# Optimization experiments

Measured on AMD Instinct MI355X. Metric: run time of the kernel, lower is better.

The kernel has to match this reference:

```python
import jax, jax.numpy as jnp
import numpy as np

B, SEQ, C, H, L = 2, 512, 768, 12, 6
OBS = ACT = GOAL = 64
MAXEP = 1000
D = C // H
T3 = 3 * SEQ  # stacked (z, state, action) tokens per timestep


def _ln(x, g, b):
    m = jnp.mean(x, -1, keepdims=True)
    v = jnp.mean((x - m) ** 2, -1, keepdims=True)
    return (x - m) * jax.lax.rsqrt(v + 1e-5) * g + b


def setup_inputs() -> dict:
    key = jax.random.key(0)
    it = iter(jax.random.split(key, 64))
    nrm = lambda shape, s=0.02: jax.random.normal(next(it), shape, jnp.float32) * s
    z = lambda *s: jnp.zeros(s, jnp.float32)
    o = lambda *s: jnp.ones(s, jnp.float32)
    return dict(
        states=jax.random.normal(next(it), (B, SEQ, OBS), jnp.float32),
        actions=jax.random.normal(next(it), (B, SEQ, ACT), jnp.float32),
        goals=jax.random.normal(next(it), (B, 1, GOAL), jnp.float32),
        traj_mask=jnp.ones((B, SEQ), bool),
        timesteps=jax.random.randint(next(it), (B, SEQ), 0, MAXEP),
        W_s=nrm((OBS, C)), b_s=z(C),
        W_a=nrm((ACT, C)), b_a=z(C),
        W_g=nrm((GOAL, C)), b_g=z(C),
        E_t=nrm((MAXEP, C)),
        ln0_g=o(C), ln0_b=z(C),
        Wq=nrm((L, C, C)), bq=z(L, C),
        Wk=nrm((L, C, C)), bk=z(L, C),
        Wv=nrm((L, C, C)), bv=z(L, C),
        Wp=nrm((L, C, C)), bp=z(L, C),
        ln1_g=o(L, C), ln1_b=z(L, C),
        W1=nrm((L, C, 4 * C)), b1=z(L, 4 * C),
        W2=nrm((L, 4 * C, C)), b2=z(L, C),
        ln2_g=o(L, C), ln2_b=z(L, C),
        W_ps=nrm((C, OBS)), b_ps=z(OBS),
        W_pa=nrm((C, ACT)), b_pa=z(ACT),
    )


def _forward(states, actions, goals, timesteps,
             W_s, b_s, W_a, b_a, W_g, b_g, E_t, ln0_g, ln0_b,
             Wq, bq, Wk, bk, Wv, bv, Wp, bp, ln1_g, ln1_b,
             W1, b1, W2, b2, ln2_g, ln2_b, W_ps, b_ps, W_pa, b_pa):
    te = E_t[timesteps]  # [B,SEQ,C] time embeddings (use_pe_as_timestep path)
    s_emb = states @ W_s + b_s + te
    a_emb = actions @ W_a + b_a + te
    g = jnp.broadcast_to(goals, (goals.shape[0], SEQ, goals.shape[2]))
    z_emb = g @ W_g + b_g + te  # GOAL_CONDITION path
    # interleave (z, s, a) per timestep -> [B, 3*SEQ, C]
    x = jnp.stack((z_emb, s_emb, a_emb), axis=2).reshape(states.shape[0], T3, C)
    x = _ln(x, ln0_g, ln0_b)
    mask = jnp.tril(jnp.ones((T3, T3), bool))
    scale = 1.0 / np.sqrt(D)
    for l in range(L):
        q = (x @ Wq[l] + bq[l]).reshape(-1, T3, H, D)
        k = (x @ Wk[l] + bk[l]).reshape(-1, T3, H, D)
        v = (x @ Wv[l] + bv[l]).reshape(-1, T3, H, D)
        sc = jnp.einsum('bqhd,bkhd->bhqk', q, k) * scale
        sc = jnp.where(mask, sc, -jnp.inf)
        w = jax.nn.softmax(sc, axis=-1)
        att = jnp.einsum('bhqk,bkhd->bqhd', w, v).reshape(-1, T3, C)
        x = x + att @ Wp[l] + bp[l]
        x = _ln(x, ln1_g[l], ln1_b[l])
        h = jax.nn.gelu(x @ W1[l] + b1[l], approximate=False)
        x = x + h @ W2[l] + b2[l]
        x = _ln(x, ln2_g[l], ln2_b[l])
    x = x.reshape(-1, SEQ, 3, C)
    state_preds = x[:, :, 2] @ W_ps + b_ps     # read off action-token positions
    action_preds = jnp.tanh(x[:, :, 1] @ W_pa + b_pa)  # state-token positions
    return jnp.stack((state_preds, action_preds))  # [2,B,SEQ,64]


def reference(states, actions, goals, traj_mask, timesteps,
              W_s, b_s, W_a, b_a, W_g, b_g, E_t, ln0_g, ln0_b,
              Wq, bq, Wk, bk, Wv, bv, Wp, bp, ln1_g, ln1_b,
              W1, b1, W2, b2, ln2_g, ln2_b, W_ps, b_ps, W_pa, b_pa):
    del traj_mask  # unused on the GOAL_CONDITION path
    return _forward(states, actions, goals, timesteps,
                    W_s, b_s, W_a, b_a, W_g, b_g, E_t, ln0_g, ln0_b,
                    Wq, bq, Wk, bk, Wv, bv, Wp, bp, ln1_g, ln1_b,
                    W1, b1, W2, b2, ln2_g, ln2_b, W_ps, b_ps, W_pa, b_pa)
```

## Files before the change

### kernel.cpp

```cpp
#include <hip/hip_runtime.h>

#define SEQ 512
#define T3 1536
#define CDIM 768
#define NH 12
#define HD 64
#define NL 6

typedef __attribute__((ext_vector_type(8))) short bh8;
typedef __attribute__((ext_vector_type(4))) short s4;
typedef __attribute__((ext_vector_type(4))) float f4;

__device__ inline short f2bf(float f) {
    union { float f; unsigned u; } x; x.f = f;
    unsigned r = x.u + 0x7FFFu + ((x.u >> 16) & 1u);
    return (short)(r >> 16);
}

__device__ inline float bf2f(short s) {
    union { unsigned u; float f; } x;
    x.u = ((unsigned)(unsigned short)s) << 16;
    return x.f;
}

__device__ inline void gload16(const short* g, const short* l) {
    __builtin_amdgcn_global_load_lds(
        (const __attribute__((address_space(1))) unsigned int*)g,
        (__attribute__((address_space(3))) unsigned int*)l, 16, 0, 0);
}

__device__ inline float block_sum(float v, volatile float* red, int tid) {
    #pragma unroll
    for (int off = 32; off > 0; off >>= 1) v += __shfl_down(v, off, 64);
    __syncthreads();
    if ((tid & 63) == 0) red[tid >> 6] = v;
    __syncthreads();
    return red[0] + red[1] + red[2] + red[3];
}

__global__ __launch_bounds__(256) void conv64_k(
        const float* __restrict__ Wq, const float* __restrict__ Wk,
        const float* __restrict__ Wv, const float* __restrict__ Wp,
        const float* __restrict__ W1, const float* __restrict__ W2,
        short* __restrict__ dst, int l0) {
    int flat = blockIdx.x;
    int lrel = flat / 1728, r = flat - lrel * 1728;
    int l = l0 + lrel;
    short* dstL = dst + (size_t)lrel * 7077888;
    const float* src; short* d; int K, N, tk, tn;
    if (r < 576) {
        int mat = r / 144, t = r - mat * 144;
        tk = t / 12; tn = t % 12; K = 768; N = 768;
        const float* srcs[4] = {Wq, Wk, Wv, Wp};
        src = srcs[mat] + (size_t)l * 589824;
        d = dstL + mat * 589824;
    } else if (r < 1152) {
        int t = r - 576; tk = t / 48; tn = t % 48; K = 768; N = 3072;
        src = W1 + (size_t)l * 2359296; d = dstL + 2359296;
    } else {
        int t = r - 1152; tk = t / 12; tn = t % 12; K = 3072; N = 768;
        src = W2 + (size_t)l * 2359296; d = dstL + 4718592;
    }
    int k0 = tk * 64, n0 = tn * 64;
    __shared__ float t2[64][65];
    int tid = threadIdx.x;
    int rk = tid >> 4, cn4 = (tid & 15) * 4;
    #pragma unroll
    for (int p = 0; p < 4; ++p) {
        f4 v = *(const f4*)(src + (size_t)(k0 + p * 16 + rk) * N + n0 + cn4);
        #pragma unroll
        for (int j = 0; j < 4; ++j) t2[cn4 + j][p * 16 + rk] = v[j];
    }
    __syncthreads();
    int n = tid >> 2, kb = (tid & 3) * 16;
    bh8 o0, o1;
    #pragma unroll
    for (int j = 0; j < 8; ++j) o0[j] = f2bf(t2[n][kb + j]);
    #pragma unroll
    for (int j = 0; j < 8; ++j) o1[j] = f2bf(t2[n][kb + 8 + j]);
    short* wp = d + (size_t)(n0 + n) * K + k0 + kb;
    *(bh8*)wp = o0;
    *(bh8*)(wp + 8) = o1;
}

__global__ __launch_bounds__(256) void embed_ln0_k(
        const float* __restrict__ states, const float* __restrict__ actions,
        const float* __restrict__ goals, const int* __restrict__ timesteps,
        const float* __restrict__ W_s, const float* __restrict__ b_s,
        const float* __restrict__ W_a, const float* __restrict__ b_a,
        const float* __restrict__ W_g, const float* __restrict__ b_g,
        const float* __restrict__ E_t, const float* __restrict__ g0,
        const float* __restrict__ bb0, float* __restrict__ x, short* __restrict__ xb) {
    int row = blockIdx.x;
    int b = row / T3, t3 = row - b * T3;
    int t = t3 / 3, kind = t3 - t * 3;
    __shared__ float inv[64];
    __shared__ float xr[CDIM];
    __shared__ float red[4];
    int tid = threadIdx.x;
    const float* src; const float* W; const float* bias;
    if (kind == 0)      { src = goals + b * 64;                       W = W_g; bias = b_g; }
    else if (kind == 1) { src = states + ((size_t)b * SEQ + t) * 64;  W = W_s; bias = b_s; }
    else                { src = actions + ((size_t)b * SEQ + t) * 64; W = W_a; bias = b_a; }
    if (tid < 64) inv[tid] = src[tid];
    __syncthreads();
    int ts = timesteps[b * SEQ + t];
    for (int c = tid; c < CDIM; c += 256) {
        float acc = bias[c] + E_t[(size_t)ts * CDIM + c];
        #pragma unroll 8
        for (int kk = 0; kk < 64; ++kk) acc += inv[kk] * W[kk * CDIM + c];
        xr[c] = acc;
    }
    __syncthreads();
    float v0 = xr[tid], v1 = xr[tid + 256], v2 = xr[tid + 512];
    float mean = block_sum(v0 + v1 + v2, red, tid) * (1.f / CDIM);
    float d0 = v0 - mean, d1 = v1 - mean, d2 = v2 - mean;
    float var = block_sum(d0 * d0 + d1 * d1 + d2 * d2, red, tid) * (1.f / CDIM);
    float rs = rsqrtf(var + 1e-5f);
    float* w = x + (size_t)row * CDIM;
    short* wb = xb + (size_t)row * CDIM;
    float o0 = d0 * rs * g0[tid]       + bb0[tid];
    float o1 = d1 * rs * g0[tid + 256] + bb0[tid + 256];
    float o2 = d2 * rs * g0[tid + 512] + bb0[tid + 512];
    w[tid] = o0; w[tid + 256] = o1; w[tid + 512] = o2;
    wb[tid] = f2bf(o0); wb[tid + 256] = f2bf(o1); wb[tid + 512] = f2bf(o2);
}

__global__ __launch_bounds__(256) void ln_k(float* __restrict__ x, short* __restrict__ outb,
                                            const float* __restrict__ g, const float* __restrict__ bb) {
    int row = blockIdx.x, tid = threadIdx.x;
    __shared__ float red[4];
    float* r = x + (size_t)row * CDIM;
    float v0 = r[tid], v1 = r[tid + 256], v2 = r[tid + 512];
    float mean = block_sum(v0 + v1 + v2, red, tid) * (1.f / CDIM);
    float d0 = v0 - mean, d1 = v1 - mean, d2 = v2 - mean;
    float var = block_sum(d0 * d0 + d1 * d1 + d2 * d2, red, tid) * (1.f / CDIM);
    float rs = rsqrtf(var + 1e-5f);
    short* wb = outb + (size_t)row * CDIM;
    float o0 = d0 * rs * g[tid]       + bb[tid];
    float o1 = d1 * rs * g[tid + 256] + bb[tid + 256];
    float o2 = d2 * rs * g[tid + 512] + bb[tid + 512];
    r[tid] = o0; r[tid + 256] = o1; r[tid + 512] = o2;
    wb[tid] = f2bf(o0); wb[tid + 256] = f2bf(o1); wb[tid + 512] = f2bf(o2);
}

template<int BM, int EPI>
__global__ __launch_bounds__(256) void gemm4_k(
        const short* __restrict__ A, const short* __restrict__ B0,
        const short* __restrict__ B1, const short* __restrict__ B2,
        const float* __restrict__ bias0, const float* __restrict__ bias1,
        const float* __restrict__ bias2,
        float* __restrict__ outF, short* __restrict__ outQ,
        short* __restrict__ outK, short* __restrict__ outV,
        int N, int K) {
    const short* Bw = B0; const float* bias = bias0; short* outB = outQ;
    int zid = 0;
    if (EPI == 0) {
        zid = blockIdx.z;
        if (zid == 1) { Bw = B1; bias = bias1; outB = outK; }
        else if (zid == 2) { Bw = B2; bias = bias2; outB = outV; }
    }
    __shared__ short As[2][BM * 64];
    __shared__ short Bs[2][128 * 64];
    int tid = threadIdx.x, lane = tid & 63, wave = tid >> 6;
    int wm = wave >> 1, wn = wave & 1, lr = lane & 15, lg = lane >> 4;
    int bm = blockIdx.y * BM, bn = blockIdx.x * 128;
    int rl = lane >> 3, ch = (lane & 7) ^ rl;
    constexpr int MI = BM / 32;

    auto STAGE = [&](int k0, int buf) {
        #pragma unroll
        for (int j = 0; j < BM / 32; ++j)
            gload16(A + (size_t)(bm + wave * (BM / 4) + j * 8 + rl) * K + k0 + ch * 8,
                    &As[buf][(wave * (BM / 4) + j * 8) * 64]);
        #pragma unroll
        for (int j = 0; j < 4; ++j)
            gload16(Bw + (size_t)(bn + wave * 32 + j * 8 + rl) * K + k0 + ch * 8,
                    &Bs[buf][(wave * 32 + j * 8) * 64]);
    };

    f4 acc[MI][4] = {};
    STAGE(0, 0);
    int cur = 0;
    for (int k0 = 0; k0 < K; k0 += 64) {
        if (k0 + 64 < K) {
            STAGE(k0 + 64, cur ^ 1);
            if constexpr (BM == 128) asm volatile("s_waitcnt vmcnt(8)" ::: "memory");
            else                     asm volatile("s_waitcnt vmcnt(6)" ::: "memory");
        } else {
            asm volatile("s_waitcnt vmcnt(0)" ::: "memory");
        }
        __builtin_amdgcn_s_barrier();
        __builtin_amdgcn_sched_barrier(0);
        bh8 af[MI][2], bf[4][2];
        #pragma unroll
        for (int mi = 0; mi < MI; ++mi)
        #pragma unroll
        for (int kk = 0; kk < 2; ++kk) {
            int m = wm * (BM / 2) + mi * 16 + lr;
            af[mi][kk] = *(const bh8*)(&As[cur][m * 64 + (((kk * 4 + lg) ^ (lr & 7)) * 8)]);
        }
        #pragma unroll
        for (int ni = 0; ni < 4; ++ni)
        #pragma unroll
        for (int kk = 0; kk < 2; ++kk) {
            int n = wn * 64 + ni * 16 + lr;
            bf[ni][kk] = *(const bh8*)(&Bs[cur][n * 64 + (((kk * 4 + lg) ^ (lr & 7)) * 8)]);
        }
        #pragma unroll
        for (int kk = 0; kk < 2; ++kk)
        #pragma unroll
        for (int mi = 0; mi < MI; ++mi)
        #pragma unroll
        for (int ni = 0; ni < 4; ++ni)
            acc[mi][ni] = __builtin_amdgcn_mfma_f32_16x16x32_bf16(af[mi][kk], bf[ni][kk], acc[mi][ni], 0, 0, 0);
        __builtin_amdgcn_sched_barrier(0);
        __builtin_amdgcn_s_barrier();
        cur ^= 1;
    }
    #pragma unroll
    for (int mi = 0; mi < MI; ++mi)
    #pragma unroll
    for (int ni = 0; ni < 4; ++ni)
    #pragma unroll
    for (int i = 0; i < 4; ++i) {
        int row = bm + wm * (BM / 2) + mi * 16 + lg * 4 + i;
        int col = bn + wn * 64 + ni * 16 + lr;
        float vv = acc[mi][ni][i] + bias[col];
        if (EPI == 0) {
            int b = row / T3, t = row - b * T3;
            int h = col >> 6, d = col & 63;
            if (zid == 2) outB[((size_t)(b * NH + h) * 64 + d) * T3 + t] = f2bf(vv);
            else          outB[((((size_t)b * NH + h) * T3 + t) << 6) + d] = f2bf(vv);
        } else if (EPI == 1) {
            size_t idx = (size_t)row * N + col;
            outF[idx] = vv + outF[idx];
        } else {
            float gl = 0.5f * vv * (1.0f + erff(vv * 0.70710678118f));
            outQ[(size_t)row * N + col] = f2bf(gl);
        }
    }
}

__global__ __launch_bounds__(256) void attn_k(const short* __restrict__ q, const short* __restrict__ k,
                                              const short* __restrict__ vt, short* __restrict__ att) {
    int idx = blockIdx.x;
    int qt = 23 - (idx / 24);
    int bh = idx % 24;
    int b = bh / NH, h = bh - b * NH;
    const short* qb = q  + (size_t)bh * T3 * HD;
    const short* kb = k  + (size_t)bh * T3 * HD;
    const short* vb = vt + (size_t)bh * HD * T3;
    __shared__ short Ks[2][4096];
    __shared__ short Vs[2][4096];
    __shared__ short Pl[4][16][72];
    int tid = threadIdx.x, lane = tid & 63, wave = tid >> 6;
    int lr = lane & 15, lg = lane >> 4;
    int rl = lane >> 3, ch = (lane & 7) ^ rl;
    int qrow0 = qt * 64 + wave * 16;
    bh8 aq0 = *(const bh8*)(qb + (size_t)(qrow0 + lr) * HD + lg * 8);
    bh8 aq1 = *(const bh8*)(qb + (size_t)(qrow0 + lr) * HD + 32 + lg * 8);
    f4 o[4] = {};
    float lsum[4] = {0.f, 0.f, 0.f, 0.f};

    auto STAGE = [&](int kt2, int buf) {
        const short* kb2 = kb + (size_t)kt2 * 64 * HD;
        #pragma unroll
        for (int j = 0; j < 2; ++j)
            gload16(kb2 + (wave * 16 + j * 8 + rl) * HD + ch * 8,
                    &Ks[buf][(wave * 16 + j * 8) * 64]);
        const short* vb2 = vb + kt2 * 64;
        #pragma unroll
        for (int j = 0; j < 2; ++j)
            gload16(vb2 + (size_t)(wave * 16 + j * 8 + rl) * T3 + ch * 8,
                    &Vs[buf][(wave * 16 + j * 8) * 64]);
    };

    STAGE(0, 0);
    int cur = 0;
    for (int kt = 0; kt <= qt; ++kt) {
        if (kt < qt) {
            STAGE(kt + 1, cur ^ 1);
            asm volatile("s_waitcnt vmcnt(4)" ::: "memory");
        } else {
            asm volatile("s_waitcnt vmcnt(0)" ::: "memory");
        }
        __builtin_amdgcn_s_barrier();
        __builtin_amdgcn_sched_barrier(0);
        const short* Kb = &Ks[cur][0];
        const short* Vb = &Vs[cur][0];
        f4 s[4];
        #pragma unroll
        for (int nf = 0; nf < 4; ++nf) {
            int tok = nf * 16 + lr;
            bh8 bk0 = *(const bh8*)(Kb + tok * 64 + ((lg ^ (lr & 7)) * 8));
            bh8 bk1 = *(const bh8*)(Kb + tok * 64 + (((4 + lg) ^ (lr & 7)) * 8));
            f4 t = {};
            t = __builtin_amdgcn_mfma_f32_16x16x32_bf16(aq0, bk0, t, 0, 0, 0);
            t = __builtin_amdgcn_mfma_f32_16x16x32_bf16(aq1, bk1, t, 0, 0, 0);
            s[nf] = t;
        }
        #pragma unroll
        for (int nf = 0; nf < 4; ++nf)
        #pragma unroll
        for (int i = 0; i < 4; ++i) {
            float p = __expf(s[nf][i] * 0.125f);
            if (kt == qt && (nf * 16 + lr) > (wave * 16 + lg * 4 + i)) p = 0.f;
            lsum[i] += p;
            Pl[wave][lg * 4 + i][nf * 16 + lr] = f2bf(p);
        }
        bh8 ap0 = *(const bh8*)&Pl[wave][lr][lg * 8];
        bh8 ap1 = *(const bh8*)&Pl[wave][lr][32 + lg * 8];
        #pragma unroll
        for (int nf = 0; nf < 4; ++nf) {
            int d = nf * 16 + lr;
            bh8 bv0 = *(const bh8*)(Vb + d * 64 + ((lg ^ (lr & 7)) * 8));
            bh8 bv1 = *(const bh8*)(Vb + d * 64 + (((4 + lg) ^ (lr & 7)) * 8));
            o[nf] = __builtin_amdgcn_mfma_f32_16x16x32_bf16(ap0, bv0, o[nf], 0, 0, 0);
            o[nf] = __builtin_amdgcn_mfma_f32_16x16x32_bf16(ap1, bv1, o[nf], 0, 0, 0);
        }
        __builtin_amdgcn_sched_barrier(0);
        __builtin_amdgcn_s_barrier();
        cur ^= 1;
    }
    float linv[4];
    #pragma unroll
    for (int i = 0; i < 4; ++i) {
        float l = lsum[i];
        #pragma unroll
        for (int off = 1; off < 16; off <<= 1) l += __shfl_xor(l, off, 16);
        linv[i] = 1.f / l;
    }
    #pragma unroll
    for (int nf = 0; nf < 4; ++nf)
    #pragma unroll
    for (int i = 0; i < 4; ++i) {
        int qrow = qrow0 + lg * 4 + i;
        att[((size_t)b * T3 + qrow) * CDIM + h * 64 + nf * 16 + lr] = f2bf(o[nf][i] * linv[i]);
    }
}

__global__ __launch_bounds__(64) void head_k(const short* __restrict__ x,
                                             const float* __restrict__ Wps, const float* __restrict__ bps,
                                             const float* __restrict__ Wpa, const float* __restrict__ bpa,
                                             float* __restrict__ out) {
    int o = blockIdx.y;
    int bs = blockIdx.x;
    int b = bs >> 9, t = bs & 511;
    int kind = (o == 0) ? 2 : 1;
    const float* W = (o == 0) ? Wps : Wpa;
    const float* bi = (o == 0) ? bps : bpa;
    const short* xr = x + ((size_t)b * T3 + t * 3 + kind) * CDIM;
    int n = threadIdx.x;
    float a0 = 0.f, a1 = 0.f, a2 = 0.f, a3 = 0.f;
    for (int kk = 0; kk < CDIM; kk += 4) {
        s4 xv = *(const s4*)(xr + kk);
        a0 = fmaf(bf2f(xv[0]), W[(kk)     * 64 + n], a0);
        a1 = fmaf(bf2f(xv[1]), W[(kk + 1) * 64 + n], a1);
        a2 = fmaf(bf2f(xv[2]), W[(kk + 2) * 64 + n], a2);
        a3 = fmaf(bf2f(xv[3]), W[(kk + 3) * 64 + n], a3);
    }
    float acc = bi[n] + ((a0 + a1) + (a2 + a3));
    if (o == 1) acc = tanhf(acc);
    out[(((size_t)o * 2 + b) * SEQ + t) * 64 + n] = acc;
}

extern "C" void kernel_launch(void* const* d_in, const int* in_sizes, int n_in,
                              void* d_out, int out_size, void* d_ws, size_t ws_size,
                              hipStream_t stream) {
    const float* states    = (const float*)d_in[0];
    const float* actions   = (const float*)d_in[1];
    const float* goals     = (const float*)d_in[2];
    const int*   timesteps = (const int*)d_in[4];
    const float* W_s = (const float*)d_in[5];  const float* b_s = (const float*)d_in[6];
    const float* W_a = (const float*)d_in[7];  const float* b_a = (const float*)d_in[8];
    const float* W_g = (const float*)d_in[9];  const float* b_g = (const float*)d_in[10];
    const float* E_t = (const float*)d_in[11];
    const float* ln0_g = (const float*)d_in[12]; const float* ln0_b = (const float*)d_in[13];
    const float* Wq = (const float*)d_in[14]; const float* bq = (const float*)d_in[15];
    const float* Wk = (const float*)d_in[16]; const float* bk = (const float*)d_in[17];
    const float* Wv = (const float*)d_in[18]; const float* bv = (const float*)d_in[19];
    const float* Wp = (const float*)d_in[20]; const float* bp = (const float*)d_in[21];
    const float* ln1_g = (const float*)d_in[22]; const float* ln1_b = (const float*)d_in[23];
    const float* W1 = (const float*)d_in[24]; const float* b1 = (const float*)d_in[25];
    const float* W2 = (const float*)d_in[26]; const float* b2 = (const float*)d_in[27];
    const float* ln2_g = (const float*)d_in[28]; const float* ln2_b = (const float*)d_in[29];
    const float* W_ps = (const float*)d_in[30]; const float* b_ps = (const float*)d_in[31];
    const float* W_pa = (const float*)d_in[32]; const float* b_pa = (const float*)d_in[33];

    char* ws = (char*)d_ws;
    float* x_f   = (float*)(ws);
    short* x_bf  = (short*)(ws + 9437184);
    short* h_bf  = (short*)(ws + 14155776);
    short* qb    = (short*)(ws + 33030144);
    short* kb    = (short*)(ws + 37748736);
    short* vbt   = (short*)(ws + 42467328);
    short* wts   = (short*)(ws + 47185920);

    const long long WL = 7077888;
    bool allw = ws_size >= 132120576ull;

    embed_ln0_k<<<dim3(2 * T3), 256, 0, stream>>>(states, actions, goals, timesteps,
        W_s, b_s, W_a, b_a, W_g, b_g, E_t, ln0_g, ln0_b, x_f, x_bf);

    if (allw)
        conv64_k<<<dim3(1728 * NL), 256, 0, stream>>>(Wq, Wk, Wv, Wp, W1, W2, wts, 0);

    for (int l = 0; l < NL; ++l) {
        size_t bo = (size_t)l * CDIM, b1o = (size_t)l * 4 * CDIM;
        if (!allw)
            conv64_k<<<dim3(1728), 256, 0, stream>>>(Wq, Wk, Wv, Wp, W1, W2, wts, l);
        short* wb  = wts + (allw ? (long long)l * WL : 0);
        short* Wqt = wb;
        short* Wkt = wb + 589824;
        short* Wvt = wb + 1179648;
        short* Wpt = wb + 1769472;
        short* W1t = wb + 2359296;
        short* W2t = wb + 4718592;

        gemm4_k<128, 0><<<dim3(6, 24, 3), 256, 0, stream>>>(x_bf, Wqt, Wkt, Wvt,
            bq + bo, bk + bo, bv + bo, nullptr, qb, kb, vbt, CDIM, CDIM);
        attn_k<<<dim3(576), 256, 0, stream>>>(qb, kb, vbt, x_bf);
        gemm4_k<64, 1><<<dim3(6, 48, 1), 256, 0, stream>>>(x_bf, Wpt, nullptr, nullptr,
            bp + bo, nullptr, nullptr, x_f, nullptr, nullptr, nullptr, CDIM, CDIM);
        ln_k<<<dim3(2 * T3), 256, 0, stream>>>(x_f, x_bf, ln1_g + bo, ln1_b + bo);
        gemm4_k<128, 2><<<dim3(24, 24, 1), 256, 0, stream>>>(x_bf, W1t, nullptr, nullptr,
            b1 + b1o, nullptr, nullptr, nullptr, h_bf, nullptr, nullptr, 4 * CDIM, CDIM);
        gemm4_k<64, 1><<<dim3(6, 48, 1), 256, 0, stream>>>(h_bf, W2t, nullptr, nullptr,
            b2 + bo, nullptr, nullptr, x_f, nullptr, nullptr, nullptr, CDIM, 4 * CDIM);
        ln_k<<<dim3(2 * T3), 256, 0, stream>>>(x_f, x_bf, ln2_g + bo, ln2_b + bo);
    }

    head_k<<<dim3(1024, 2), 64, 0, stream>>>(x_bf, W_ps, b_ps, W_pa, b_pa, (float*)d_out);
}
```

Measured before the change: 1.216 ms.

## Drop GEMM double buffering, shrink tiles, use wave-per-row LayerNorm, alias workspace

The GEMM kernel loses its LDS double buffer and explicit vmcnt pipelining in favour of a single buffer with plain __syncthreads, and gains a BN parameter. The QKV, projection and W2 GEMMs now use 64x64 tiles, giving more blocks for occupancy. LayerNorm is rewritten to handle one row per wave with shuffle reductions and a single-pass mean/variance. Q/K/V buffers now alias the h buffer so the workspace can be smaller; this gives up load/compute overlap in the GEMMs, and the single-pass variance is less numerically robust.

```diff
diff --git a/kernel.cpp b/kernel.cpp
--- a/kernel.cpp
+++ b/kernel.cpp
@@ -68,8 +68,8 @@
     #pragma unroll
     for (int p = 0; p < 4; ++p) {
         f4 v = *(const f4*)(src + (size_t)(k0 + p * 16 + rk) * N + n0 + cn4);
-        #pragma unroll
-        for (int j = 0; j < 4; ++j) t2[cn4 + j][p * 16 + rk] = v[j];
+        t2[cn4][p * 16 + rk] = v[0]; t2[cn4 + 1][p * 16 + rk] = v[1];
+        t2[cn4 + 2][p * 16 + rk] = v[2]; t2[cn4 + 3][p * 16 + rk] = v[3];
     }
     __syncthreads();
     int n = tid >> 2, kb = (tid & 3) * 16;
@@ -128,24 +128,33 @@
 
 __global__ __launch_bounds__(256) void ln_k(float* __restrict__ x, short* __restrict__ outb,
                                             const float* __restrict__ g, const float* __restrict__ bb) {
-    int row = blockIdx.x, tid = threadIdx.x;
-    __shared__ float red[4];
+    int wave = threadIdx.x >> 6, lane = threadIdx.x & 63;
+    int row = blockIdx.x * 4 + wave;
     float* r = x + (size_t)row * CDIM;
-    float v0 = r[tid], v1 = r[tid + 256], v2 = r[tid + 512];
-    float mean = block_sum(v0 + v1 + v2, red, tid) * (1.f / CDIM);
-    float d0 = v0 - mean, d1 = v1 - mean, d2 = v2 - mean;
-    float var = block_sum(d0 * d0 + d1 * d1 + d2 * d2, red, tid) * (1.f / CDIM);
+    short* wb = outb + (size_t)row * CDIM;
+    float v[12];
+    float s = 0.f, s2 = 0.f;
+    #pragma unroll
+    for (int j = 0; j < 12; ++j) {
+        v[j] = r[lane + j * 64];
+        s += v[j]; s2 += v[j] * v[j];
+    }
+    #pragma unroll
+    for (int off = 32; off > 0; off >>= 1) { s += __shfl_xor(s, off, 64); s2 += __shfl_xor(s2, off, 64); }
+    float mean = s * (1.f / CDIM);
+    float var = s2 * (1.f / CDIM) - mean * mean;
     float rs = rsqrtf(var + 1e-5f);
-    short* wb = outb + (size_t)row * CDIM;
-    float o0 = d0 * rs * g[tid]       + bb[tid];
-    float o1 = d1 * rs * g[tid + 256] + bb[tid + 256];
-    float o2 = d2 * rs * g[tid + 512] + bb[tid + 512];
-    r[tid] = o0; r[tid + 256] = o1; r[tid + 512] = o2;
-    wb[tid] = f2bf(o0); wb[tid + 256] = f2bf(o1); wb[tid + 512] = f2bf(o2);
-}
-
-template<int BM, int EPI>
-__global__ __launch_bounds__(256) void gemm4_k(
+    #pragma unroll
+    for (int j = 0; j < 12; ++j) {
+        int c = lane + j * 64;
+        float o = (v[j] - mean) * rs * g[c] + bb[c];
+        r[c] = o;
+        wb[c] = f2bf(o);
+    }
+}
+
+template<int BM, int BN, int EPI>
+__global__ __launch_bounds__(256) void gemm5_k(
         const short* __restrict__ A, const short* __restrict__ B0,
         const short* __restrict__ B1, const short* __restrict__ B2,
         const float* __restrict__ bias0, const float* __restrict__ bias1,
@@ -160,72 +169,56 @@
         if (zid == 1) { Bw = B1; bias = bias1; outB = outK; }
         else if (zid == 2) { Bw = B2; bias = bias2; outB = outV; }
     }
-    __shared__ short As[2][BM * 64];
-    __shared__ short Bs[2][128 * 64];
+    __shared__ short As[BM * 64];
+    __shared__ short Bs[BN * 64];
     int tid = threadIdx.x, lane = tid & 63, wave = tid >> 6;
     int wm = wave >> 1, wn = wave & 1, lr = lane & 15, lg = lane >> 4;
-    int bm = blockIdx.y * BM, bn = blockIdx.x * 128;
+    int bm = blockIdx.y * BM, bn = blockIdx.x * BN;
     int rl = lane >> 3, ch = (lane & 7) ^ rl;
-    constexpr int MI = BM / 32;
-
-    auto STAGE = [&](int k0, int buf) {
+    constexpr int MI = BM / 32, NI = BN / 32;
+    f4 acc[MI][NI] = {};
+    for (int k0 = 0; k0 < K; k0 += 64) {
         #pragma unroll
         for (int j = 0; j < BM / 32; ++j)
             gload16(A + (size_t)(bm + wave * (BM / 4) + j * 8 + rl) * K + k0 + ch * 8,
-                    &As[buf][(wave * (BM / 4) + j * 8) * 64]);
-        #pragma unroll
-        for (int j = 0; j < 4; ++j)
-            gload16(Bw + (size_t)(bn + wave * 32 + j * 8 + rl) * K + k0 + ch * 8,
-                    &Bs[buf][(wave * 32 + j * 8) * 64]);
-    };
-
-    f4 acc[MI][4] = {};
-    STAGE(0, 0);
-    int cur = 0;
-    for (int k0 = 0; k0 < K; k0 += 64) {
-        if (k0 + 64 < K) {
-            STAGE(k0 + 64, cur ^ 1);
-            if constexpr (BM == 128) asm volatile("s_waitcnt vmcnt(8)" ::: "memory");
-            else                     asm volatile("s_waitcnt vmcnt(6)" ::: "memory");
-        } else {
-            asm volatile("s_waitcnt vmcnt(0)" ::: "memory");
-        }
-        __builtin_amdgcn_s_barrier();
-        __builtin_amdgcn_sched_barrier(0);
-        bh8 af[MI][2], bf[4][2];
+                    As + (wave * (BM / 4) + j * 8) * 64);
+        #pragma unroll
+        for (int j = 0; j < BN / 32; ++j)
+            gload16(Bw + (size_t)(bn + wave * (BN / 4) + j * 8 + rl) * K + k0 + ch * 8,
+                    Bs + (wave * (BN / 4) + j * 8) * 64);
+        __syncthreads();
+        bh8 af[MI][2], bf[NI][2];
         #pragma unroll
         for (int mi = 0; mi < MI; ++mi)
         #pragma unroll
         for (int kk = 0; kk < 2; ++kk) {
             int m = wm * (BM / 2) + mi * 16 + lr;
-            af[mi][kk] = *(const bh8*)(&As[cur][m * 64 + (((kk * 4 + lg) ^ (lr & 7)) * 8)]);
-        }
-        #pragma unroll
-        for (int ni = 0; ni < 4; ++ni)
+            af[mi][kk] = *(const bh8*)(As + m * 64 + (((kk * 4 + lg) ^ (lr & 7)) * 8));
+        }
+        #pragma unroll
+        for (int ni = 0; ni < NI; ++ni)
         #pragma unroll
         for (int kk = 0; kk < 2; ++kk) {
-            int n = wn * 64 + ni * 16 + lr;
-            bf[ni][kk] = *(const bh8*)(&Bs[cur][n * 64 + (((kk * 4 + lg) ^ (lr & 7)) * 8)]);
+            int n = wn * (BN / 2) + ni * 16 + lr;
+            bf[ni][kk] = *(const bh8*)(Bs + n * 64 + (((kk * 4 + lg) ^ (lr & 7)) * 8));
         }
         #pragma unroll
         for (int kk = 0; kk < 2; ++kk)
         #pragma unroll
         for (int mi = 0; mi < MI; ++mi)
         #pragma unroll
-        for (int ni = 0; ni < 4; ++ni)
+        for (int ni = 0; ni < NI; ++ni)
             acc[mi][ni] = __builtin_amdgcn_mfma_f32_16x16x32_bf16(af[mi][kk], bf[ni][kk], acc[mi][ni], 0, 0, 0);
-        __builtin_amdgcn_sched_barrier(0);
-        __builtin_amdgcn_s_barrier();
-        cur ^= 1;
+        __syncthreads();
     }
     #pragma unroll
     for (int mi = 0; mi < MI; ++mi)
     #pragma unroll
-    for (int ni = 0; ni < 4; ++ni)
+    for (int ni = 0; ni < NI; ++ni)
     #pragma unroll
     for (int i = 0; i < 4; ++i) {
         int row = bm + wm * (BM / 2) + mi * 16 + lg * 4 + i;
-        int col = bn + wn * 64 + ni * 16 + lr;
+        int col = bn + wn * (BN / 2) + ni * 16 + lr;
         float vv = acc[mi][ni][i] + bias[col];
         if (EPI == 0) {
             int b = row / T3, t = row - b * T3;
@@ -392,13 +385,13 @@
     float* x_f   = (float*)(ws);
     short* x_bf  = (short*)(ws + 9437184);
     short* h_bf  = (short*)(ws + 14155776);
-    short* qb    = (short*)(ws + 33030144);
-    short* kb    = (short*)(ws + 37748736);
-    short* vbt   = (short*)(ws + 42467328);
-    short* wts   = (short*)(ws + 47185920);
+    short* qb    = (short*)(ws + 14155776);
+    short* kb    = (short*)(ws + 18874368);
+    short* vbt   = (short*)(ws + 23592960);
+    short* wts   = (short*)(ws + 33030144);
 
     const long long WL = 7077888;
-    bool allw = ws_size >= 132120576ull;
+    bool allw = ws_size >= 117964800ull;
 
     embed_ln0_k<<<dim3(2 * T3), 256, 0, stream>>>(states, actions, goals, timesteps,
         W_s, b_s, W_a, b_a, W_g, b_g, E_t, ln0_g, ln0_b, x_f, x_bf);
@@ -418,17 +411,17 @@
         short* W1t = wb + 2359296;
         short* W2t = wb + 4718592;
 
-        gemm4_k<128, 0><<<dim3(6, 24, 3), 256, 0, stream>>>(x_bf, Wqt, Wkt, Wvt,
+        gemm5_k<64, 64, 0><<<dim3(12, 48, 3), 256, 0, stream>>>(x_bf, Wqt, Wkt, Wvt,
             bq + bo, bk + bo, bv + bo, nullptr, qb, kb, vbt, CDIM, CDIM);
         attn_k<<<dim3(576), 256, 0, stream>>>(qb, kb, vbt, x_bf);
-        gemm4_k<64, 1><<<dim3(6, 48, 1), 256, 0, stream>>>(x_bf, Wpt, nullptr, nullptr,
+        gemm5_k<64, 64, 1><<<dim3(12, 48, 1), 256, 0, stream>>>(x_bf, Wpt, nullptr, nullptr,
             bp + bo, nullptr, nullptr, x_f, nullptr, nullptr, nullptr, CDIM, CDIM);
-        ln_k<<<dim3(2 * T3), 256, 0, stream>>>(x_f, x_bf, ln1_g + bo, ln1_b + bo);
-        gemm4_k<128, 2><<<dim3(24, 24, 1), 256, 0, stream>>>(x_bf, W1t, nullptr, nullptr,
+        ln_k<<<dim3(768), 256, 0, stream>>>(x_f, x_bf, ln1_g + bo, ln1_b + bo);
+        gemm5_k<128, 128, 2><<<dim3(24, 24, 1), 256, 0, stream>>>(x_bf, W1t, nullptr, nullptr,
             b1 + b1o, nullptr, nullptr, nullptr, h_bf, nullptr, nullptr, 4 * CDIM, CDIM);
-        gemm4_k<64, 1><<<dim3(6, 48, 1), 256, 0, stream>>>(h_bf, W2t, nullptr, nullptr,
+        gemm5_k<64, 64, 1><<<dim3(12, 48, 1), 256, 0, stream>>>(h_bf, W2t, nullptr, nullptr,
             b2 + bo, nullptr, nullptr, x_f, nullptr, nullptr, nullptr, CDIM, 4 * CDIM);
-        ln_k<<<dim3(2 * T3), 256, 0, stream>>>(x_f, x_bf, ln2_g + bo, ln2_b + bo);
+        ln_k<<<dim3(768), 256, 0, stream>>>(x_f, x_bf, ln2_g + bo, ln2_b + bo);
     }
 
     head_k<<<dim3(1024, 2), 64, 0, stream>>>(x_bf, W_ps, b_ps, W_pa, b_pa, (float*)d_out);
```

New measurement: 1.130 ms. 7.1% less time.
